# Kernel tuning notes

Measured on AMD Instinct MI355X. Metric: run time of the kernel, lower is better.

## Reference

```python
import jax, jax.numpy as jnp
import numpy as np

T = 32          # chain length (init arg)
K = 2048        # particles per timestep (Ks)
RES = 0.5       # observed scalar (init buffer)
LIKE_STD = 1.0  # likelihood std (init arg)
LOG2PI = float(np.log(2.0 * np.pi))


def _logpdf(x, mu, std):
    # Normal(mu, std).log_prob(x)
    z = (x - mu) / std
    return -0.5 * z * z - jnp.log(std) - 0.5 * LOG2PI


def logmmmeanexp(X, Y):
    # log( exp(X) @ exp(Y) / X.shape[1] ), numerically stabilized exactly as the torch code
    x = jnp.max(X, axis=1, keepdims=True)
    y = jnp.max(Y, axis=0, keepdims=True)
    return x + y + jnp.log(jnp.exp(X - x) @ jnp.exp(Y - y)) - jnp.log(jnp.asarray(X.shape[1], X.dtype))


def setup_inputs() -> dict:
    key = jax.random.key(0)
    eps = jax.random.normal(key, (T, K), dtype=jnp.float32)
    means = jnp.zeros((T,), jnp.float32)
    # matches the torch init: sqrt((1+arange(T))/T)
    log_stds = jnp.sqrt((1.0 + jnp.arange(T, dtype=jnp.float32)) / T)
    return {"means": means, "log_stds": log_stds, "eps": eps}


def reference(means, log_stds, eps):
    std = jnp.exp(log_stds)                            # proposal stds, (T,)
    zs = means[:, None] + std[:, None] * eps           # reparameterized samples, (T,K)
    log_q = _logpdf(zs, means[:, None], std[:, None])  # proposal log-probs, (T,K)
    sp = jnp.sqrt(1.0 / T)                             # prior/transition std

    # first factor: prior over z_0 minus proposal, (1,K)
    r0 = (_logpdf(zs[0], 0.0, sp) - log_q[0])[None, :]
    # middle factors: transition log-probs, (T-1, K, K); Ms[i][j,k] = logN(zs[i+1,k]; zs[i,j], sp) - log_q[i+1,k]
    Ms = _logpdf(zs[1:, None, :], zs[:-1, :, None], sp) - log_q[1:, None, :]

    def step(r, M):
        return logmmmeanexp(r, M), None

    r, _ = jax.lax.scan(step, r0, Ms)
    # likelihood factor, (K,1)
    L = _logpdf(jnp.float32(RES), zs[-1][:, None], jnp.float32(LIKE_STD))
    return logmmmeanexp(r, L)  # (1,1) log marginal-likelihood estimate
```

## Files before the change

kernel.cpp:

```cpp
#include <hip/hip_runtime.h>
#include <math.h>

#define T 32
#define K 2048
#define NBLOCKS 256
#define NTHREADS 512
#define HB 128
#define CPB 16
#define QS 4
#define L2E_F 1.4426950408889634f
#define LN2_F 0.6931471805599453f
#define LOG2PI_F 1.8378770664093453f
#define LOG_K_F  7.6246189861593985f
#define SP_F     0.17677669529663687f
#define LOG_SP_F (-1.7328679513998633f)
#define CNORM_F  (-(LOG_SP_F) - 0.5f * LOG2PI_F)

#if __has_builtin(__builtin_amdgcn_exp2f)
#define EXP2F(x) __builtin_amdgcn_exp2f(x)
#else
#define EXP2F(x) exp2f(x)
#endif
#if __has_builtin(__builtin_amdgcn_logf)
#define LOG2F(x) __builtin_amdgcn_logf(x)
#else
#define LOG2F(x) log2f(x)
#endif

__device__ __forceinline__ float aload4(const float* p) {
    return __hip_atomic_load(p, __ATOMIC_RELAXED, __HIP_MEMORY_SCOPE_AGENT);
}
__device__ __forceinline__ void astore4(float* p, float v) {
    __hip_atomic_store(p, v, __ATOMIC_RELAXED, __HIP_MEMORY_SCOPE_AGENT);
}
__device__ __forceinline__ int sload(const int* p) {
    return __hip_atomic_load(p, __ATOMIC_RELAXED, __HIP_MEMORY_SCOPE_AGENT);
}
__device__ __forceinline__ void sstore(int* p, int v) {
    __hip_atomic_store(p, v, __ATOMIC_RELAXED, __HIP_MEMORY_SCOPE_AGENT);
}

__global__ __launch_bounds__(NTHREADS) void fused_kernel(
    const float* __restrict__ means, const float* __restrict__ log_stds,
    const float* __restrict__ eps, float* __restrict__ fbuf,
    float* __restrict__ bbuf, int* __restrict__ fsent, int* __restrict__ bsent,
    float* __restrict__ out)
{
    __shared__ float2 shzD[2][K];
    __shared__ float2 lzc[T][CPB];
    __shared__ float smu[T], sstd[T], slq2[T];
    __shared__ float red[NTHREADS];
    __shared__ int ldsflag;

    const int tid  = threadIdx.x;
    const int b    = blockIdx.x;
    const bool fwd = (b < HB);
    const int lb   = fwd ? b : b - HB;
    const int col0 = lb * CPB;

    if (tid == 0) ldsflag = 0;

    {
        int t = tid >> 4, dcol = tid & 15;
        float mu = means[t];
        float st = expf(log_stds[t]);
        if (dcol == 0) {
            smu[t] = mu; sstd[t] = st;
            slq2[t] = L2E_F * (logf(st) + 0.5f * LOG2PI_F);
        }
        float e = eps[t * K + col0 + dcol];
        float z = fmaf(st, e, mu);
        float log_q = fmaf(-0.5f * e, e, -logf(st) - 0.5f * LOG2PI_F);
        float tz2 = (32.0f * L2E_F) * z;
        if (fwd) {
            float cm2 = fmaf((-16.0f * L2E_F) * z, z,
                             L2E_F * (CNORM_F - log_q)) - 11.0f;
            lzc[t][dcol] = make_float2(tz2, cm2);
            if (t == 0) {
                float r0 = fmaf(-16.0f * z, z, CNORM_F) - log_q;
                astore4(&fbuf[col0 + dcol], r0 * L2E_F);
            }
        } else {
            float cm2 = fmaf((-16.0f * L2E_F) * z, z, L2E_F * CNORM_F) - 11.0f;
            lzc[t][dcol] = make_float2(tz2, cm2);
            if (t == T - 1) {
                float d = 0.5f - z;
                float c31 = fmaf(-0.5f * d, d, -0.5f * LOG2PI_F);
                astore4(&bbuf[col0 + dcol], c31 * L2E_F);
            }
        }
    }
    __syncthreads();
    int* mysent = fwd ? fsent : bsent;
    if (tid == 0) sstore(&mysent[lb], 1);

    const int lane = tid & 63;
    const int wave = tid >> 6;
    float* mybuf = fwd ? fbuf : bbuf;
    const int nstep = fwd ? 16 : 15;

    for (int p = 0; p < nstep; ++p) {
        const int par = p & 1;
        const int need = p + 1;
        const int tin  = fwd ? p : 31 - p;
        const int town = fwd ? p + 1 : 30 - p;
        const float mu_i  = smu[tin];
        const float std_i = sstd[tin];
        const float lqc   = slq2[tin];
        const float* erow = eps + tin * K;

        float zloc[QS], dadd[QS];
        #pragma unroll
        for (int q = 0; q < QS; ++q) {
            float e = erow[tid + q * NTHREADS];
            float z = fmaf(std_i, e, mu_i);
            zloc[q] = z;
            float base = fwd ? 0.0f : fmaf((0.5f * L2E_F) * e, e, lqc);
            dadd[q] = fmaf((-16.0f * L2E_F) * z, z, base);
        }

        if (wave == 0) {
            for (;;) {
                int v0 = sload(&mysent[lane]);
                int v1 = sload(&mysent[lane + 64]);
                if (__all(min(v0, v1) >= need)) break;
                __builtin_amdgcn_s_sleep(1);
            }
            __hip_atomic_store(&ldsflag, need, __ATOMIC_RELEASE,
                               __HIP_MEMORY_SCOPE_WORKGROUP);
        } else {
            while (__hip_atomic_load(&ldsflag, __ATOMIC_ACQUIRE,
                                     __HIP_MEMORY_SCOPE_WORKGROUP) < need)
                __builtin_amdgcn_s_sleep(1);
        }

        const float* mrow = mybuf + par * K;
        float rv[QS];
        #pragma unroll
        for (int q = 0; q < QS; ++q) rv[q] = aload4(&mrow[tid + q * NTHREADS]);
        #pragma unroll
        for (int q = 0; q < QS; ++q)
            shzD[par][tid + q * NTHREADS] = make_float2(zloc[q], rv[q] + dadd[q]);
        __syncthreads();

        const float4* shp = (const float4*)&shzD[par][0];
        float2 zcA = lzc[town][2 * wave];
        float2 zcB = lzc[town][2 * wave + 1];
        float4 fr[16];
        #pragma unroll
        for (int i = 0; i < 16; ++i) fr[i] = shp[lane + (i << 6)];
        float m0 = -INFINITY, m1 = -INFINITY;
        #pragma unroll
        for (int i = 0; i < 16; ++i) {
            m0 = fmaxf(m0, fmaxf(fmaf(zcA.x, fr[i].x, fr[i].y),
                                 fmaf(zcA.x, fr[i].z, fr[i].w)));
            m1 = fmaxf(m1, fmaxf(fmaf(zcB.x, fr[i].x, fr[i].y),
                                 fmaf(zcB.x, fr[i].z, fr[i].w)));
        }
        #pragma unroll
        for (int off = 32; off >= 1; off >>= 1) {
            m0 = fmaxf(m0, __shfl_xor(m0, off, 64));
            m1 = fmaxf(m1, __shfl_xor(m1, off, 64));
        }
        float s0 = 0.0f, s1 = 0.0f;
        #pragma unroll
        for (int i = 0; i < 16; ++i) {
            s0 += EXP2F(fmaf(zcA.x, fr[i].x, fr[i].y) - m0);
            s0 += EXP2F(fmaf(zcA.x, fr[i].z, fr[i].w) - m0);
            s1 += EXP2F(fmaf(zcB.x, fr[i].x, fr[i].y) - m1);
            s1 += EXP2F(fmaf(zcB.x, fr[i].z, fr[i].w) - m1);
        }
        #pragma unroll
        for (int off = 32; off >= 1; off >>= 1) {
            s0 += __shfl_xor(s0, off, 64);
            s1 += __shfl_xor(s1, off, 64);
        }
        if (lane < 2) {
            float mm = lane ? m1 : m0;
            float sv = lane ? s1 : s0;
            float cm = lane ? zcB.y : zcA.y;
            astore4(&mybuf[(par ^ 1) * K + col0 + 2 * wave + lane],
                    cm + mm + LOG2F(sv));
        }
        __syncthreads();
        if (tid == 0) sstore(&mysent[lb], p + 2);
    }

    if (b == 0) {
        for (;;) {
            int f0 = sload(&fsent[lane]);
            int f1 = sload(&fsent[lane + 64]);
            int b0 = sload(&bsent[lane]);
            int b1 = sload(&bsent[lane + 64]);
            bool ok = (min(f0, f1) >= 17) && (min(b0, b1) >= 16);
            if (__all(ok)) break;
            __builtin_amdgcn_s_sleep(1);
        }
        const float* rrow = fbuf + 0 * K;
        const float* crow = bbuf + 1 * K;
        float vals[QS];
        float m = -INFINITY;
        #pragma unroll
        for (int q = 0; q < QS; ++q) {
            int j = tid + q * NTHREADS;
            float v = aload4(&rrow[j]) + aload4(&crow[j]);
            vals[q] = v;
            m = fmaxf(m, v);
        }
        red[tid] = m; __syncthreads();
        for (int off = NTHREADS / 2; off >= 1; off >>= 1) {
            if (tid < off) red[tid] = fmaxf(red[tid], red[tid + off]);
            __syncthreads();
        }
        m = red[0]; __syncthreads();
        float ssum = 0.0f;
        #pragma unroll
        for (int q = 0; q < QS; ++q) ssum += EXP2F(vals[q] - m);
        red[tid] = ssum; __syncthreads();
        for (int off = NTHREADS / 2; off >= 1; off >>= 1) {
            if (tid < off) red[tid] += red[tid + off];
            __syncthreads();
        }
        if (tid == 0)
            out[0] = LN2_F * (m + LOG2F(red[0]) - 11.0f);
    }
}

extern "C" void kernel_launch(void* const* d_in, const int* in_sizes, int n_in,
                              void* d_out, int out_size, void* d_ws, size_t ws_size,
                              hipStream_t stream) {
    const float* means    = (const float*)d_in[0];
    const float* log_stds = (const float*)d_in[1];
    const float* eps      = (const float*)d_in[2];
    float* out = (float*)d_out;

    float* fbuf = (float*)d_ws;
    float* bbuf = fbuf + 2 * K;
    int*   fsent = (int*)(bbuf + 2 * K);
    int*   bsent = fsent + 128;

    fused_kernel<<<NBLOCKS, NTHREADS, 0, stream>>>(
        means, log_stds, eps, fbuf, bbuf, fsent, bsent, out);
}
```

Baseline: 119.9 us.

## Replace per-block sentinels with tagged value slots and per-wave LDS chunk flags

Each inter-block value is now stored as a 64-bit pair of value and step tag, so consumers poll the data slots directly instead of separate sentinel counters. Block-wide __syncthreads is replaced by per-wave chunk-ready and done flags in LDS, and the block grows to 1024 threads so each wave computes one output column. The aim is to remove the sentinel round trip and the barrier latency from each step of the 16-step chain. The cost is more spin-waiting in LDS and register pressure from the 32-entry fragment array at 1024 threads. Stale tags in the workspace from a previous launch could also be mistaken for fresh data.

Result: slower. 167.3 us (+39.6%).

```diff
diff --git a/kernel.cpp b/kernel.cpp
--- a/kernel.cpp
+++ b/kernel.cpp
@@ -4,10 +4,10 @@
 #define T 32
 #define K 2048
 #define NBLOCKS 256
-#define NTHREADS 512
+#define NTHREADS 1024
+#define NWAVES 16
 #define HB 128
 #define CPB 16
-#define QS 4
 #define L2E_F 1.4426950408889634f
 #define LN2_F 0.6931471805599453f
 #define LOG2PI_F 1.8378770664093453f
@@ -27,30 +27,30 @@
 #define LOG2F(x) log2f(x)
 #endif
 
-__device__ __forceinline__ float aload4(const float* p) {
-    return __hip_atomic_load(p, __ATOMIC_RELAXED, __HIP_MEMORY_SCOPE_AGENT);
-}
-__device__ __forceinline__ void astore4(float* p, float v) {
-    __hip_atomic_store(p, v, __ATOMIC_RELAXED, __HIP_MEMORY_SCOPE_AGENT);
-}
-__device__ __forceinline__ int sload(const int* p) {
-    return __hip_atomic_load(p, __ATOMIC_RELAXED, __HIP_MEMORY_SCOPE_AGENT);
-}
-__device__ __forceinline__ void sstore(int* p, int v) {
-    __hip_atomic_store(p, v, __ATOMIC_RELAXED, __HIP_MEMORY_SCOPE_AGENT);
+union Pack { float2 f; unsigned long long u; };
+__device__ __forceinline__ float2 aload8(const float2* p) {
+    Pack pk;
+    pk.u = __hip_atomic_load((const unsigned long long*)p,
+                             __ATOMIC_RELAXED, __HIP_MEMORY_SCOPE_AGENT);
+    return pk.f;
+}
+__device__ __forceinline__ void astore8(float2* p, float v, int tag) {
+    Pack pk; pk.f.x = v; pk.f.y = __int_as_float(tag);
+    __hip_atomic_store((unsigned long long*)p, pk.u,
+                       __ATOMIC_RELAXED, __HIP_MEMORY_SCOPE_AGENT);
 }
 
 __global__ __launch_bounds__(NTHREADS) void fused_kernel(
     const float* __restrict__ means, const float* __restrict__ log_stds,
-    const float* __restrict__ eps, float* __restrict__ fbuf,
-    float* __restrict__ bbuf, int* __restrict__ fsent, int* __restrict__ bsent,
-    float* __restrict__ out)
+    const float* __restrict__ eps, float2* __restrict__ fbuf,
+    float2* __restrict__ bbuf, float* __restrict__ out)
 {
     __shared__ float2 shzD[2][K];
     __shared__ float2 lzc[T][CPB];
     __shared__ float smu[T], sstd[T], slq2[T];
     __shared__ float red[NTHREADS];
-    __shared__ int ldsflag;
+    __shared__ int chunkflag[2][NWAVES];
+    __shared__ int donef[2][NWAVES];
 
     const int tid  = threadIdx.x;
     const int b    = blockIdx.x;
@@ -58,9 +58,10 @@
     const int lb   = fwd ? b : b - HB;
     const int col0 = lb * CPB;
 
-    if (tid == 0) ldsflag = 0;
-
-    {
+    if (tid < 2 * NWAVES)      ((int*)chunkflag)[tid] = 0;
+    else if (tid < 4 * NWAVES) ((int*)donef)[tid - 2 * NWAVES] = 0;
+
+    if (tid < T * CPB) {
         int t = tid >> 4, dcol = tid & 15;
         float mu = means[t];
         float st = expf(log_stds[t]);
@@ -78,7 +79,7 @@
             lzc[t][dcol] = make_float2(tz2, cm2);
             if (t == 0) {
                 float r0 = fmaf(-16.0f * z, z, CNORM_F) - log_q;
-                astore4(&fbuf[col0 + dcol], r0 * L2E_F);
+                astore8(&fbuf[col0 + dcol], r0 * L2E_F, 1);
             }
         } else {
             float cm2 = fmaf((-16.0f * L2E_F) * z, z, L2E_F * CNORM_F) - 11.0f;
@@ -86,143 +87,132 @@
             if (t == T - 1) {
                 float d = 0.5f - z;
                 float c31 = fmaf(-0.5f * d, d, -0.5f * LOG2PI_F);
-                astore4(&bbuf[col0 + dcol], c31 * L2E_F);
+                astore8(&bbuf[col0 + dcol], c31 * L2E_F, 1);
             }
         }
     }
     __syncthreads();
-    int* mysent = fwd ? fsent : bsent;
-    if (tid == 0) sstore(&mysent[lb], 1);
 
     const int lane = tid & 63;
     const int wave = tid >> 6;
-    float* mybuf = fwd ? fbuf : bbuf;
+    float2* mybuf = fwd ? fbuf : bbuf;
     const int nstep = fwd ? 16 : 15;
+    const int j0 = wave * 128 + lane;
+    const int j1 = j0 + 64;
 
     for (int p = 0; p < nstep; ++p) {
-        const int par = p & 1;
-        const int need = p + 1;
+        const int par  = p & 1;
+        const int tg   = p + 1;
         const int tin  = fwd ? p : 31 - p;
         const int town = fwd ? p + 1 : 30 - p;
         const float mu_i  = smu[tin];
         const float std_i = sstd[tin];
         const float lqc   = slq2[tin];
-        const float* erow = eps + tin * K;
-
-        float zloc[QS], dadd[QS];
-        #pragma unroll
-        for (int q = 0; q < QS; ++q) {
-            float e = erow[tid + q * NTHREADS];
-            float z = fmaf(std_i, e, mu_i);
-            zloc[q] = z;
-            float base = fwd ? 0.0f : fmaf((0.5f * L2E_F) * e, e, lqc);
-            dadd[q] = fmaf((-16.0f * L2E_F) * z, z, base);
-        }
-
-        if (wave == 0) {
+
+        float e0 = eps[tin * K + j0];
+        float e1 = eps[tin * K + j1];
+        float z0 = fmaf(std_i, e0, mu_i);
+        float z1 = fmaf(std_i, e1, mu_i);
+        float b0 = fwd ? 0.0f : fmaf((0.5f * L2E_F) * e0, e0, lqc);
+        float b1 = fwd ? 0.0f : fmaf((0.5f * L2E_F) * e1, e1, lqc);
+        float d0 = fmaf((-16.0f * L2E_F) * z0, z0, b0);
+        float d1 = fmaf((-16.0f * L2E_F) * z1, z1, b1);
+
+        {
+            const int need = p - 1;
             for (;;) {
-                int v0 = sload(&mysent[lane]);
-                int v1 = sload(&mysent[lane + 64]);
-                if (__all(min(v0, v1) >= need)) break;
-                __builtin_amdgcn_s_sleep(1);
-            }
-            __hip_atomic_store(&ldsflag, need, __ATOMIC_RELEASE,
-                               __HIP_MEMORY_SCOPE_WORKGROUP);
-        } else {
-            while (__hip_atomic_load(&ldsflag, __ATOMIC_ACQUIRE,
-                                     __HIP_MEMORY_SCOPE_WORKGROUP) < need)
-                __builtin_amdgcn_s_sleep(1);
-        }
-
-        const float* mrow = mybuf + par * K;
-        float rv[QS];
-        #pragma unroll
-        for (int q = 0; q < QS; ++q) rv[q] = aload4(&mrow[tid + q * NTHREADS]);
-        #pragma unroll
-        for (int q = 0; q < QS; ++q)
-            shzD[par][tid + q * NTHREADS] = make_float2(zloc[q], rv[q] + dadd[q]);
+                int v = (lane < NWAVES)
+                    ? __hip_atomic_load(&donef[par][lane], __ATOMIC_ACQUIRE,
+                                        __HIP_MEMORY_SCOPE_WORKGROUP)
+                    : 0x7fffffff;
+                if (__all(v >= need)) break;
+            }
+        }
+
+        float2* mrow = mybuf + par * K;
+        float2 v0 = aload8(&mrow[j0]);
+        float2 v1 = aload8(&mrow[j1]);
+        while (!__all((__float_as_int(v0.y) == tg) &
+                      (__float_as_int(v1.y) == tg))) {
+            __builtin_amdgcn_s_sleep(1);
+            if (__float_as_int(v0.y) != tg) v0 = aload8(&mrow[j0]);
+            if (__float_as_int(v1.y) != tg) v1 = aload8(&mrow[j1]);
+        }
+
+        shzD[par][j0] = make_float2(z0, v0.x + d0);
+        shzD[par][j1] = make_float2(z1, v1.x + d1);
+        __hip_atomic_store(&chunkflag[par][wave], tg, __ATOMIC_RELEASE,
+                           __HIP_MEMORY_SCOPE_WORKGROUP);
+
+        float2 zc = lzc[town][wave];
+        float tz2 = zc.x, cm2 = zc.y;
+        float2 fr[32];
+        float mM = -INFINITY;
+        #pragma unroll
+        for (int i = 0; i < 16; ++i) {
+            int cw = (wave + i) & 15;
+            if (i > 0) {
+                while (__hip_atomic_load(&chunkflag[par][cw], __ATOMIC_ACQUIRE,
+                                         __HIP_MEMORY_SCOPE_WORKGROUP) < tg) {}
+            }
+            float2 a = shzD[par][cw * 128 + lane];
+            float2 c = shzD[par][cw * 128 + 64 + lane];
+            fr[2 * i]     = a;
+            fr[2 * i + 1] = c;
+            mM = fmaxf(mM, fmaxf(fmaf(tz2, a.x, a.y), fmaf(tz2, c.x, c.y)));
+        }
+        __hip_atomic_store(&donef[par][wave], tg, __ATOMIC_RELEASE,
+                           __HIP_MEMORY_SCOPE_WORKGROUP);
+
+        #pragma unroll
+        for (int off = 32; off >= 1; off >>= 1)
+            mM = fmaxf(mM, __shfl_xor(mM, off, 64));
+        float ss = 0.0f;
+        #pragma unroll
+        for (int i = 0; i < 32; ++i)
+            ss += EXP2F(fmaf(tz2, fr[i].x, fr[i].y) - mM);
+        #pragma unroll
+        for (int off = 32; off >= 1; off >>= 1)
+            ss += __shfl_xor(ss, off, 64);
+
+        if (lane == 0)
+            astore8(&mybuf[(par ^ 1) * K + col0 + wave],
+                    cm2 + mM + LOG2F(ss), p + 2);
+    }
+
+    if (b == 0) {
         __syncthreads();
-
-        const float4* shp = (const float4*)&shzD[par][0];
-        float2 zcA = lzc[town][2 * wave];
-        float2 zcB = lzc[town][2 * wave + 1];
-        float4 fr[16];
-        #pragma unroll
-        for (int i = 0; i < 16; ++i) fr[i] = shp[lane + (i << 6)];
-        float m0 = -INFINITY, m1 = -INFINITY;
-        #pragma unroll
-        for (int i = 0; i < 16; ++i) {
-            m0 = fmaxf(m0, fmaxf(fmaf(zcA.x, fr[i].x, fr[i].y),
-                                 fmaf(zcA.x, fr[i].z, fr[i].w)));
-            m1 = fmaxf(m1, fmaxf(fmaf(zcB.x, fr[i].x, fr[i].y),
-                                 fmaf(zcB.x, fr[i].z, fr[i].w)));
-        }
-        #pragma unroll
-        for (int off = 32; off >= 1; off >>= 1) {
-            m0 = fmaxf(m0, __shfl_xor(m0, off, 64));
-            m1 = fmaxf(m1, __shfl_xor(m1, off, 64));
-        }
-        float s0 = 0.0f, s1 = 0.0f;
-        #pragma unroll
-        for (int i = 0; i < 16; ++i) {
-            s0 += EXP2F(fmaf(zcA.x, fr[i].x, fr[i].y) - m0);
-            s0 += EXP2F(fmaf(zcA.x, fr[i].z, fr[i].w) - m0);
-            s1 += EXP2F(fmaf(zcB.x, fr[i].x, fr[i].y) - m1);
-            s1 += EXP2F(fmaf(zcB.x, fr[i].z, fr[i].w) - m1);
-        }
-        #pragma unroll
-        for (int off = 32; off >= 1; off >>= 1) {
-            s0 += __shfl_xor(s0, off, 64);
-            s1 += __shfl_xor(s1, off, 64);
-        }
-        if (lane < 2) {
-            float mm = lane ? m1 : m0;
-            float sv = lane ? s1 : s0;
-            float cm = lane ? zcB.y : zcA.y;
-            astore4(&mybuf[(par ^ 1) * K + col0 + 2 * wave + lane],
-                    cm + mm + LOG2F(sv));
-        }
-        __syncthreads();
-        if (tid == 0) sstore(&mysent[lb], p + 2);
-    }
-
-    if (b == 0) {
+        const int jA = tid, jB = tid + NTHREADS;
+        float2 a0 = aload8(&fbuf[jA]);
+        float2 a1 = aload8(&fbuf[jB]);
+        float2 c0 = aload8(&bbuf[K + jA]);
+        float2 c1 = aload8(&bbuf[K + jB]);
         for (;;) {
-            int f0 = sload(&fsent[lane]);
-            int f1 = sload(&fsent[lane + 64]);
-            int b0 = sload(&bsent[lane]);
-            int b1 = sload(&bsent[lane + 64]);
-            bool ok = (min(f0, f1) >= 17) && (min(b0, b1) >= 16);
+            bool ok = (__float_as_int(a0.y) == 17) & (__float_as_int(a1.y) == 17)
+                    & (__float_as_int(c0.y) == 16) & (__float_as_int(c1.y) == 16);
             if (__all(ok)) break;
             __builtin_amdgcn_s_sleep(1);
-        }
-        const float* rrow = fbuf + 0 * K;
-        const float* crow = bbuf + 1 * K;
-        float vals[QS];
-        float m = -INFINITY;
-        #pragma unroll
-        for (int q = 0; q < QS; ++q) {
-            int j = tid + q * NTHREADS;
-            float v = aload4(&rrow[j]) + aload4(&crow[j]);
-            vals[q] = v;
-            m = fmaxf(m, v);
-        }
+            if (__float_as_int(a0.y) != 17) a0 = aload8(&fbuf[jA]);
+            if (__float_as_int(a1.y) != 17) a1 = aload8(&fbuf[jB]);
+            if (__float_as_int(c0.y) != 16) c0 = aload8(&bbuf[K + jA]);
+            if (__float_as_int(c1.y) != 16) c1 = aload8(&bbuf[K + jB]);
+        }
+        float vA = a0.x + c0.x;
+        float vB = a1.x + c1.x;
+        float m = fmaxf(vA, vB);
         red[tid] = m; __syncthreads();
         for (int off = NTHREADS / 2; off >= 1; off >>= 1) {
             if (tid < off) red[tid] = fmaxf(red[tid], red[tid + off]);
             __syncthreads();
         }
         m = red[0]; __syncthreads();
-        float ssum = 0.0f;
-        #pragma unroll
-        for (int q = 0; q < QS; ++q) ssum += EXP2F(vals[q] - m);
+        float ssum = EXP2F(vA - m) + EXP2F(vB - m);
         red[tid] = ssum; __syncthreads();
         for (int off = NTHREADS / 2; off >= 1; off >>= 1) {
             if (tid < off) red[tid] += red[tid + off];
             __syncthreads();
         }
-        if (tid == 0)
-            out[0] = LN2_F * (m + LOG2F(red[0]) - 11.0f);
+        if (tid == 0) out[0] = LN2_F * (m + LOG2F(red[0]) - 11.0f);
     }
 }
 
@@ -234,11 +224,9 @@
     const float* eps      = (const float*)d_in[2];
     float* out = (float*)d_out;
 
-    float* fbuf = (float*)d_ws;
-    float* bbuf = fbuf + 2 * K;
-    int*   fsent = (int*)(bbuf + 2 * K);
-    int*   bsent = fsent + 128;
+    float2* fbuf = (float2*)d_ws;
+    float2* bbuf = fbuf + 2 * K;
 
     fused_kernel<<<NBLOCKS, NTHREADS, 0, stream>>>(
-        means, log_stds, eps, fbuf, bbuf, fsent, bsent, out);
-}
+        means, log_stds, eps, fbuf, bbuf, out);
+}
```
